# Kernel optimization log

Measured on AMD Instinct MI355X. Metric: run time of the kernel, lower is better.

## Reference

```python
import jax, jax.numpy as jnp
import numpy as np
import math

B, T, C, H = 8, 1024, 1024, 16
HS = C // H  # head size 64
FF = 4 * C
EPS = 1e-5


def quant_weight(W, e, b):
    """Fake-quant with straight-through rounding, per QLinear.forward.
    W:[...,out,in], e:[...,out,1], b:[...,out,1] -> effective weight 2**e * round_ste(clip(2**-e * W))."""
    b_rel = jax.nn.relu(b)
    mn = jnp.where(b_rel > 0, -(2.0 ** (b_rel - 1)), 0.0)
    mx = jnp.where(b_rel > 0, 2.0 ** (b_rel - 1) - 1.0, 0.0)
    qw = jnp.clip((2.0 ** (-e)) * W, mn, mx)
    w = qw + jax.lax.stop_gradient(jnp.round(qw) - qw)  # STE round
    return (2.0 ** e) * w


def layer_norm(x, g, beta):
    mu = jnp.mean(x, axis=-1, keepdims=True)
    var = jnp.mean((x - mu) ** 2, axis=-1, keepdims=True)
    return (x - mu) * jax.lax.rsqrt(var + EPS) * g + beta


def _uniform(key, shape, fan_in):
    s = 1.0 / math.sqrt(fan_in)
    return jax.random.uniform(key, shape, jnp.float32, -s, s)


def setup_inputs() -> dict:
    key = jax.random.key(0)
    ks = jax.random.split(key, 8)
    d = {"x": jax.random.normal(ks[0], (B, T, C), jnp.float32)}
    # stacked per-head QKV QLinear params (bias=False)
    d["Wq"] = _uniform(ks[1], (H, HS, C), C)
    d["Wk"] = _uniform(ks[2], (H, HS, C), C)
    d["Wv"] = _uniform(ks[3], (H, HS, C), C)
    for n in ("q", "k", "v"):
        d["e" + n] = jnp.full((H, HS, 1), -8.0, jnp.float32)
        d["b" + n] = jnp.full((H, HS, 1), 32.0, jnp.float32)
    # output projection QLinear (bias=True)
    d["Wp"] = _uniform(ks[4], (C, C), C)
    d["ep"] = jnp.full((C, 1), -8.0, jnp.float32)
    d["bp"] = jnp.full((C, 1), 32.0, jnp.float32)
    d["biasp"] = jnp.zeros((C,), jnp.float32)
    # FFN QLinears
    d["W1"] = _uniform(ks[5], (FF, C), C)
    d["e1"] = jnp.full((FF, 1), -8.0, jnp.float32)
    d["b1"] = jnp.full((FF, 1), 32.0, jnp.float32)
    d["bias1"] = jnp.zeros((FF,), jnp.float32)
    d["W2"] = _uniform(ks[6], (C, FF), FF)
    d["e2"] = jnp.full((C, 1), -8.0, jnp.float32)
    d["b2"] = jnp.full((C, 1), 32.0, jnp.float32)
    d["bias2"] = jnp.zeros((C,), jnp.float32)
    # LayerNorms
    d["g1"] = jnp.ones((C,), jnp.float32)
    d["be1"] = jnp.zeros((C,), jnp.float32)
    d["g2"] = jnp.ones((C,), jnp.float32)
    d["be2"] = jnp.zeros((C,), jnp.float32)
    return d


def block_forward(x, Wq, eq, bq, Wk, ek, bk, Wv, ev, bv,
                  Wp, ep, bp, biasp, W1, e1, b1, bias1, W2, e2, b2, bias2,
                  g1, be1, g2, be2):
    h = layer_norm(x, g1, be1)
    q = jnp.einsum('btc,hdc->bhtd', h, quant_weight(Wq, eq, bq))
    k = jnp.einsum('btc,hdc->bhtd', h, quant_weight(Wk, ek, bk))
    v = jnp.einsum('btc,hdc->bhtd', h, quant_weight(Wv, ev, bv))
    # NOTE: source scales by C**-0.5 where C = n_embd (not head_size)
    wei = jnp.einsum('bhtd,bhsd->bhts', q, k) * (C ** -0.5)
    causal = jnp.tril(jnp.ones((T, T), bool))
    wei = jnp.where(causal, wei, -jnp.inf)
    wei = jax.nn.softmax(wei, axis=-1)
    att = jnp.einsum('bhts,bhsd->bhtd', wei, v)  # [B,H,T,HS]
    att = att.transpose(0, 2, 1, 3).reshape(B, T, C)  # concat heads
    x = x + att @ quant_weight(Wp, ep, bp).T + biasp
    h2 = layer_norm(x, g2, be2)
    f = jax.nn.relu(h2 @ quant_weight(W1, e1, b1).T + bias1)
    f = f @ quant_weight(W2, e2, b2).T + bias2
    return x + f


def reference(x, Wq, eq, bq, Wk, ek, bk, Wv, ev, bv,
              Wp, ep, bp, biasp, W1, e1, b1, bias1, W2, e2, b2, bias2,
              g1, be1, g2, be2):
    return block_forward(x, Wq, eq, bq, Wk, ek, bk, Wv, ev, bv,
                         Wp, ep, bp, biasp, W1, e1, b1, bias1, W2, e2, b2, bias2,
                         g1, be1, g2, be2)
```

## Files before the change

### kernel.cpp

```cpp
#include <hip/hip_runtime.h>
#include <hip/hip_bf16.h>
#include <math.h>

#define DEVI __device__ __forceinline__

typedef __attribute__((ext_vector_type(8))) short bf16x8;
typedef __attribute__((ext_vector_type(4))) float f32x4;

DEVI unsigned short f2bf(float f) {
    union { float f; unsigned u; } v; v.f = f;
    unsigned r = v.u + 0x7FFFu + ((v.u >> 16) & 1u);
    return (unsigned short)(r >> 16);
}

DEVI unsigned cvtpk(float lo, float hi) {
    unsigned d;
    asm volatile("v_cvt_pk_bf16_f32 %0, %1, %2" : "=v"(d) : "v"(lo), "v"(hi));
    return d;
}

DEVI void gload16(const void* g, void* l) {
    __builtin_amdgcn_global_load_lds((const __attribute__((address_space(1))) void*)g,
                                     (__attribute__((address_space(3))) void*)l, 16, 0, 0);
}

#define WAITVM8() asm volatile("s_waitcnt vmcnt(8)" ::: "memory")
#define WAITVM4() asm volatile("s_waitcnt vmcnt(4)" ::: "memory")
#define WAITVM0() asm volatile("s_waitcnt vmcnt(0)" ::: "memory")
#define WAITLG0() asm volatile("s_waitcnt lgkmcnt(0)" ::: "memory")
#define WAITLG8() asm volatile("s_waitcnt lgkmcnt(8)" ::: "memory")
#define BAR()     __builtin_amdgcn_s_barrier()
#define SB()      __builtin_amdgcn_sched_barrier(0)

__global__ __launch_bounds__(256) void quant6_kernel(
    const float* __restrict__ Wq, const float* __restrict__ Wk, const float* __restrict__ Wv,
    const float* __restrict__ Wp, const float* __restrict__ W1, const float* __restrict__ W2,
    const float* __restrict__ eq, const float* __restrict__ ek, const float* __restrict__ ev,
    const float* __restrict__ ep, const float* __restrict__ e1, const float* __restrict__ e2,
    const float* __restrict__ bq, const float* __restrict__ bk, const float* __restrict__ bv,
    const float* __restrict__ bp, const float* __restrict__ b1, const float* __restrict__ b2,
    unsigned short* __restrict__ Wqkvq, unsigned short* __restrict__ Wpq,
    unsigned short* __restrict__ W1q, unsigned short* __restrict__ W2q)
{
    const int M1 = 1 << 20;
    const int NCH = 3 * M1;
    for (int c = blockIdx.x * blockDim.x + threadIdx.x; c < NCH; c += gridDim.x * blockDim.x) {
        int elem = c * 4;
        const float *W, *e, *b; unsigned short* o; int lgK, local;
        if (elem < M1)            { W = Wq; e = eq; b = bq; o = Wqkvq;          lgK = 10; local = elem; }
        else if (elem < 2 * M1)   { W = Wk; e = ek; b = bk; o = Wqkvq + M1;     lgK = 10; local = elem - M1; }
        else if (elem < 3 * M1)   { W = Wv; e = ev; b = bv; o = Wqkvq + 2 * M1; lgK = 10; local = elem - 2 * M1; }
        else if (elem < 4 * M1)   { W = Wp; e = ep; b = bp; o = Wpq;            lgK = 10; local = elem - 3 * M1; }
        else if (elem < 8 * M1)   { W = W1; e = e1; b = b1; o = W1q;            lgK = 10; local = elem - 4 * M1; }
        else                      { W = W2; e = e2; b = b2; o = W2q;            lgK = 12; local = elem - 8 * M1; }
        int row = local >> lgK;
        float evv = e[row], bvv = b[row];
        float br = fmaxf(bvv, 0.f);
        float mn, mx;
        if (br > 0.f) { float p = exp2f(br - 1.f); mn = -p; mx = p - 1.f; }
        else          { mn = 0.f; mx = 0.f; }
        float si = exp2f(-evv), so = exp2f(evv);
        union { float4 v4; float a[4]; } v;
        v.v4 = *(const float4*)(W + local);
        union { unsigned short u[4]; unsigned long long ll; } ot;
        #pragma unroll
        for (int j = 0; j < 4; j++) {
            float qw = fminf(fmaxf(si * v.a[j], mn), mx);
            ot.u[j] = f2bf(so * rintf(qw));
        }
        *(unsigned long long*)(o + local) = ot.ll;
    }
}

__global__ __launch_bounds__(256) void ln_kernel(
    const float* __restrict__ x, const float* __restrict__ g, const float* __restrict__ be,
    unsigned short* __restrict__ out)
{
    int row = blockIdx.x;
    union { float4 v4; float a[4]; } v;
    v.v4 = ((const float4*)(x + (size_t)row * 1024))[threadIdx.x];
    float s = v.a[0] + v.a[1] + v.a[2] + v.a[3];
    float s2 = v.a[0]*v.a[0] + v.a[1]*v.a[1] + v.a[2]*v.a[2] + v.a[3]*v.a[3];
    #pragma unroll
    for (int off = 32; off > 0; off >>= 1) { s += __shfl_down(s, off); s2 += __shfl_down(s2, off); }
    __shared__ float ps[4], ps2[4];
    int wave = threadIdx.x >> 6, lane = threadIdx.x & 63;
    if (lane == 0) { ps[wave] = s; ps2[wave] = s2; }
    __syncthreads();
    float mu = (ps[0] + ps[1] + ps[2] + ps[3]) * (1.0f / 1024.0f);
    float var = (ps2[0] + ps2[1] + ps2[2] + ps2[3]) * (1.0f / 1024.0f) - mu * mu;
    float rs = rsqrtf(var + 1e-5f);
    int c = threadIdx.x * 4;
    union { unsigned short u[4]; unsigned long long ll; } o;
    #pragma unroll
    for (int j = 0; j < 4; j++) o.u[j] = f2bf((v.a[j] - mu) * rs * g[c + j] + be[c + j]);
    *(unsigned long long*)(out + (size_t)row * 1024 + c) = o.ll;
}

#define GSTAGE(buf, kt) do { \
    _Pragma("unroll") for (int q_ = 0; q_ < 4; q_++) { \
        int idx_ = q_ * 256 + tid; int row_ = idx_ >> 3; int gs_ = (idx_ & 7) ^ (row_ & 7); \
        gload16(A  + (size_t)(brow + row_) * K + (kt) * 64 + gs_ * 8, &As[buf][idx_ * 8]); \
        gload16(Bw + (size_t)(bcol + row_) * K + (kt) * 64 + gs_ * 8, &Bs[buf][idx_ * 8]); \
    } } while (0)

template<int EP>
__global__ __launch_bounds__(256) void gemm_bt(
    const unsigned short* __restrict__ A, const unsigned short* __restrict__ Bw,
    int N, int K,
    const float* __restrict__ bias, const float* __restrict__ res,
    float* __restrict__ outf, unsigned short* __restrict__ outb)
{
    __shared__ __align__(16) unsigned short As[2][128 * 64];
    __shared__ __align__(16) unsigned short Bs[2][128 * 64];
    int tid = threadIdx.x, lane = tid & 63, wave = tid >> 6;
    int gx = gridDim.x;
    int nwg = gx * gridDim.y;
    int id = blockIdx.y * gx + blockIdx.x;
    int swz = (id & 7) * (nwg >> 3) + (id >> 3);
    int brow = (swz / gx) * 128, bcol = (swz % gx) * 128;
    int wr = wave >> 1, wc = wave & 1;
    int r = lane & 15, g4 = lane >> 4;
    f32x4 acc[4][4];
    #pragma unroll
    for (int i = 0; i < 4; i++)
        #pragma unroll
        for (int j = 0; j < 4; j++) acc[i][j] = (f32x4){0.f, 0.f, 0.f, 0.f};

    int nt = K >> 6;
    GSTAGE(0, 0);
    __syncthreads();
    int cur = 0;
    for (int t = 0; t < nt; ++t) {
        if (t + 1 < nt) { GSTAGE(cur ^ 1, t + 1); WAITVM8(); }
        else            { WAITVM0(); }
        __builtin_amdgcn_s_barrier();
        #pragma unroll
        for (int kk = 0; kk < 2; kk++) {
            bf16x8 af[4], bfr[4];
            #pragma unroll
            for (int mi = 0; mi < 4; mi++) {
                int rh = wr * 64 + mi * 16 + r;
                af[mi] = *(const bf16x8*)&As[cur][rh * 64 + (((kk * 4 + g4) ^ (rh & 7)) << 3)];
            }
            #pragma unroll
            for (int ni = 0; ni < 4; ni++) {
                int rh = wc * 64 + ni * 16 + r;
                bfr[ni] = *(const bf16x8*)&Bs[cur][rh * 64 + (((kk * 4 + g4) ^ (rh & 7)) << 3)];
            }
            #pragma unroll
            for (int mi = 0; mi < 4; mi++)
                #pragma unroll
                for (int ni = 0; ni < 4; ni++)
                    acc[mi][ni] = __builtin_amdgcn_mfma_f32_16x16x32_bf16(af[mi], bfr[ni], acc[mi][ni], 0, 0, 0);
        }
        __builtin_amdgcn_s_barrier();
        cur ^= 1;
    }

    #pragma unroll
    for (int mi = 0; mi < 4; mi++)
        #pragma unroll
        for (int ni = 0; ni < 4; ni++)
            #pragma unroll
            for (int i = 0; i < 4; i++) {
                int row = brow + wr * 64 + mi * 16 + g4 * 4 + i;
                int col = bcol + wc * 64 + ni * 16 + r;
                float v = acc[mi][ni][i];
                if (EP == 0) {
                    outb[(size_t)row * N + col] = f2bf(v);
                } else if (EP == 1) {
                    outf[(size_t)row * N + col] = v + bias[col] + res[(size_t)row * N + col];
                } else {
                    outb[(size_t)row * N + col] = f2bf(fmaxf(v + bias[col], 0.f));
                }
            }
}

#define STAGE_A(b, h, kt) do { \
    _Pragma("unroll") \
    for (int ld = 0; ld < 2; ld++) { \
        int idx = ld * 512 + tid; int rw = idx >> 3; int gs = (idx & 7) ^ (rw & 7); \
        gload16(Aa + (size_t)(brow + (h) * 128 + rw) * K + (kt) * 64 + gs * 8, &As[b][h][idx * 8]); \
    } } while (0)

#define STAGE_B(b, h, kt) do { \
    _Pragma("unroll") \
    for (int ld = 0; ld < 2; ld++) { \
        int idx = ld * 512 + tid; int rw = idx >> 3; int gs = (idx & 7) ^ (rw & 7); \
        gload16(Bw + (size_t)(bcol + (h) * 128 + rw) * K + (kt) * 64 + gs * 8, &Bs[b][h][idx * 8]); \
    } } while (0)

#define RD_A(b, mh) do { \
    _Pragma("unroll") for (int mi = 0; mi < 4; mi++) \
    _Pragma("unroll") for (int kk = 0; kk < 2; kk++) { \
        int rh = (mh) * 64 + mi * 16 + r; \
        af[mi][kk] = *(const bf16x8*)&As[b][wr][rh * 64 + (((kk * 4 + g4) ^ (rh & 7)) << 3)]; \
    } } while (0)

#define RD_B2(b, nh) do { \
    _Pragma("unroll") for (int nj = 0; nj < 2; nj++) \
    _Pragma("unroll") for (int kk = 0; kk < 2; kk++) { \
        int rh = (wc & 1) * 64 + ((nh) * 2 + nj) * 16 + r; \
        bfr[(nh) * 2 + nj][kk] = *(const bf16x8*)&Bs[b][wc >> 1][rh * 64 + (((kk * 4 + g4) ^ (rh & 7)) << 3)]; \
    } } while (0)

#define QUAD(mh, nh) do { \
    __builtin_amdgcn_s_setprio(1); \
    _Pragma("unroll") for (int mi = 0; mi < 4; mi++) \
    _Pragma("unroll") for (int nj = 0; nj < 2; nj++) \
    _Pragma("unroll") for (int kk = 0; kk < 2; kk++) \
        acc[(mh) * 4 + mi][(nh) * 2 + nj] = __builtin_amdgcn_mfma_f32_16x16x32_bf16( \
            af[mi][kk], bfr[(nh) * 2 + nj][kk], acc[(mh) * 4 + mi][(nh) * 2 + nj], 0, 0, 0); \
    __builtin_amdgcn_s_setprio(0); \
    } while (0)

template<int EP>
__global__ __launch_bounds__(512, 2) void gemm256(
    const unsigned short* __restrict__ Aa, const unsigned short* __restrict__ Bw,
    int N, int K,
    const float* __restrict__ bias, const float* __restrict__ res,
    float* __restrict__ outf, unsigned short* __restrict__ outb)
{
    __shared__ __align__(16) unsigned short As[2][2][128 * 64];
    __shared__ __align__(16) unsigned short Bs[2][2][128 * 64];
    int tid = threadIdx.x, lane = tid & 63, wave = tid >> 6;
    int gx = gridDim.x;
    int nwg = gx * gridDim.y;
    int id = blockIdx.y * gx + blockIdx.x;
    int swz = (id & 7) * (nwg >> 3) + (id >> 3);
    int brow = (swz / gx) * 256, bcol = (swz % gx) * 256;
    int wr = wave >> 2, wc = wave & 3;
    int r = lane & 15, g4 = lane >> 4;
    int KT = K >> 6;

    f32x4 acc[8][4];
    #pragma unroll
    for (int i = 0; i < 8; i++)
        #pragma unroll
        for (int j = 0; j < 4; j++) acc[i][j] = (f32x4){0.f, 0.f, 0.f, 0.f};
    bf16x8 af[4][2], bfr[4][2];

    STAGE_A(0, 0, 0); STAGE_A(0, 1, 0); STAGE_B(0, 0, 0); STAGE_B(0, 1, 0);
    STAGE_B(1, 0, 1); STAGE_B(1, 1, 1);
    WAITVM4();
    BAR();

    for (int t = 0; t < KT; t += 2) {
        RD_A(0, 0); RD_B2(0, 0);
        STAGE_A(1, 0, t + 1);
        WAITLG8();
        BAR(); WAITLG0(); SB();
        QUAD(0, 0);
        BAR();
        RD_B2(0, 1);
        STAGE_A(1, 1, t + 1);
        BAR(); WAITLG0(); SB();
        QUAD(0, 1);
        BAR();
        RD_A(0, 1);
        if (t + 2 < KT) STAGE_B(0, 0, t + 2);
        BAR(); WAITLG0(); SB();
        QUAD(1, 1);
        BAR();
        if (t + 2 < KT) { STAGE_B(0, 1, t + 2); WAITVM4(); } else { WAITVM0(); }
        BAR(); WAITLG0(); SB();
        QUAD(1, 0);
        BAR();
        RD_A(1, 0); RD_B2(1, 0);
        if (t + 2 < KT) STAGE_A(0, 0, t + 2);
        WAITLG8();
        BAR(); WAITLG0(); SB();
        QUAD(0, 0);
        BAR();
        RD_B2(1, 1);
        if (t + 2 < KT) STAGE_A(0, 1, t + 2);
        BAR(); WAITLG0(); SB();
        QUAD(0, 1);
        BAR();
        RD_A(1, 1);
        if (t + 3 < KT) STAGE_B(1, 0, t + 3);
        BAR(); WAITLG0(); SB();
        QUAD(1, 1);
        BAR();
        if (t + 3 < KT) { STAGE_B(1, 1, t + 3); WAITVM4(); } else { WAITVM0(); }
        BAR(); WAITLG0(); SB();
        QUAD(1, 0);
        BAR();
    }

    #pragma unroll
    for (int m = 0; m < 8; m++)
        #pragma unroll
        for (int n = 0; n < 4; n++)
            #pragma unroll
            for (int j = 0; j < 4; j++) {
                int row = brow + wr * 128 + m * 16 + g4 * 4 + j;
                int col = bcol + wc * 64 + n * 16 + r;
                float v = acc[m][n][j];
                if (EP == 0) {
                    outb[(size_t)row * N + col] = f2bf(v);
                } else if (EP == 1) {
                    outf[(size_t)row * N + col] = v + bias[col] + res[(size_t)row * N + col];
                } else {
                    outb[(size_t)row * N + col] = f2bf(fmaxf(v + bias[col], 0.f));
                }
            }
}

__global__ __launch_bounds__(512, 4) void attn_kernel(
    const unsigned short* __restrict__ qkv, unsigned short* __restrict__ att)
{
    __shared__ __align__(16) unsigned short Ks[2][64 * 64];
    __shared__ __align__(16) unsigned short Vt[2][64 * 66];
    __shared__ __align__(16) unsigned short Ps[2][64 * 64];
    int tid = threadIdx.x, lane = tid & 63, w = tid >> 6;
    int half = w >> 2;
    int pi = blockIdx.x;
    int bh = blockIdx.y, bb = bh >> 4, hh = bh & 15;
    int r = lane & 15, g4 = lane >> 4;
    const unsigned short* base = qkv + (size_t)bb * 1024 * 3072;
    const float SCL = 0.03125f * 1.4426950408889634f;
    int vd = tid & 63, vsb = tid >> 6;
    int prow = (w & 3) * 16 + r;
    int pswz = (r & 7) << 3;

    for (int sidx = 0; sidx < 2; sidx++) {
        int s = sidx ? (7 - pi) : pi;
        int qt = 2 * s + half;
        int qtmax = 2 * s + 1;
        int qrow = qt * 64 + prow;

        bf16x8 qf[2];
        #pragma unroll
        for (int kk = 0; kk < 2; kk++)
            qf[kk] = *(const bf16x8*)&base[(size_t)qrow * 3072 + hh * 64 + kk * 32 + g4 * 8];

        f32x4 oacc[4];
        #pragma unroll
        for (int i = 0; i < 4; i++) oacc[i] = (f32x4){0.f, 0.f, 0.f, 0.f};
        float m_i = -INFINITY, l_i = 0.f;

        unsigned short vtmp[8];
        {
            int row = tid >> 3, slot = tid & 7;
            int gs = slot ^ (row & 7);
            gload16(base + (size_t)row * 3072 + 1024 + hh * 64 + gs * 8, &Ks[0][tid * 8]);
            #pragma unroll
            for (int i2 = 0; i2 < 8; i2++)
                vtmp[i2] = base[(size_t)(vsb * 8 + i2) * 3072 + 2048 + hh * 64 + vd];
            union { unsigned short u[8]; bf16x8 v; } w0;
            #pragma unroll
            for (int i2 = 0; i2 < 8; i2++) w0.u[i2] = vtmp[i2];
            *(bf16x8*)&Vt[0][vd * 66 + (vsb ^ (vd & 7)) * 8] = w0.v;
        }
        __syncthreads();

        for (int ki = 0; ki <= qtmax; ki++) {
            int cur = ki & 1;
            bool pre = (ki < qtmax);
            bool act = (ki <= qt);
            if (pre) {
                int k1 = (ki + 1) * 64;
                int row = tid >> 3, slot = tid & 7;
                int gs = slot ^ (row & 7);
                gload16(base + (size_t)(k1 + row) * 3072 + 1024 + hh * 64 + gs * 8, &Ks[cur ^ 1][tid * 8]);
                #pragma unroll
                for (int i2 = 0; i2 < 8; i2++)
                    vtmp[i2] = base[(size_t)(k1 + vsb * 8 + i2) * 3072 + 2048 + hh * 64 + vd];
            }

            if (act) {
                int k0 = ki * 64;
                f32x4 sacc[4];
                #pragma unroll
                for (int c4 = 0; c4 < 4; c4++) sacc[c4] = (f32x4){0.f, 0.f, 0.f, 0.f};
                #pragma unroll
                for (int c4 = 0; c4 < 4; c4++) {
                    int krow = c4 * 16 + r;
                    #pragma unroll
                    for (int kk = 0; kk < 2; kk++) {
                        int slot = (g4 + kk * 4) ^ (krow & 7);
                        bf16x8 kf = *(const bf16x8*)&Ks[cur][krow * 64 + slot * 8];
                        sacc[c4] = __builtin_amdgcn_mfma_f32_16x16x32_bf16(kf, qf[kk], sacc[c4], 0, 0, 0);
                    }
                }
                bool diag = (ki == qt);
                float sv[4][4];
                float smax = -INFINITY;
                #pragma unroll
                for (int c4 = 0; c4 < 4; c4++)
                    #pragma unroll
                    for (int i = 0; i < 4; i++) {
                        float sa = sacc[c4][i];
                        if (diag && (k0 + c4 * 16 + g4 * 4 + i) > qrow) sa = -INFINITY;
                        sv[c4][i] = sa;
                        smax = fmaxf(smax, sa);
                    }
                smax = fmaxf(smax, __shfl_xor(smax, 16));
                smax = fmaxf(smax, __shfl_xor(smax, 32));
                if (!__all((smax - m_i) * SCL <= 8.f)) {
                    float mn = fmaxf(m_i, smax);
                    float fs = exp2f((m_i - mn) * SCL);
                    m_i = mn;
                    l_i *= fs;
                    #pragma unroll
                    for (int n4 = 0; n4 < 4; n4++)
                        #pragma unroll
                        for (int i = 0; i < 4; i++) oacc[n4][i] *= fs;
                }
                float nb = -m_i * SCL;
                float rsum = 0.f;
                float pv[4][4];
                #pragma unroll
                for (int c4 = 0; c4 < 4; c4++)
                    #pragma unroll
                    for (int i = 0; i < 4; i++) {
                        float p = exp2f(fmaf(sv[c4][i], SCL, nb));
                        pv[c4][i] = p;
                        rsum += p;
                    }
                rsum += __shfl_xor(rsum, 16);
                rsum += __shfl_xor(rsum, 32);
                l_i += rsum;
                #pragma unroll
                for (int c4 = 0; c4 < 4; c4++) {
                    unsigned long long ll = (unsigned long long)cvtpk(pv[c4][0], pv[c4][1])
                                          | ((unsigned long long)cvtpk(pv[c4][2], pv[c4][3]) << 32);
                    *(unsigned long long*)&Ps[half][(prow * 64 + c4 * 16 + g4 * 4) ^ pswz] = ll;
                }
                WAITLG0();
            }
            if (pre) {
                union { unsigned short u[8]; bf16x8 v; } w0;
                #pragma unroll
                for (int i2 = 0; i2 < 8; i2++) w0.u[i2] = vtmp[i2];
                *(bf16x8*)&Vt[cur ^ 1][vd * 66 + (vsb ^ (vd & 7)) * 8] = w0.v;
            }
            if (act) {
                bf16x8 pa[2];
                #pragma unroll
                for (int kk = 0; kk < 2; kk++)
                    pa[kk] = *(const bf16x8*)&Ps[half][(prow * 64 + kk * 32 + g4 * 8) ^ pswz];
                #pragma unroll
                for (int n4 = 0; n4 < 4; n4++) {
                    int d = n4 * 16 + r;
                    #pragma unroll
                    for (int kk = 0; kk < 2; kk++) {
                        bf16x8 vf = *(const bf16x8*)&Vt[cur][d * 66 + (((kk * 4 + g4) ^ (d & 7)) << 3)];
                        oacc[n4] = __builtin_amdgcn_mfma_f32_16x16x32_bf16(vf, pa[kk], oacc[n4], 0, 0, 0);
                    }
                }
            }
            __syncthreads();
        }

        float inv = 1.f / l_i;
        #pragma unroll
        for (int n4 = 0; n4 < 4; n4++) {
            unsigned long long ll = (unsigned long long)cvtpk(oacc[n4][0] * inv, oacc[n4][1] * inv)
                                  | ((unsigned long long)cvtpk(oacc[n4][2] * inv, oacc[n4][3] * inv) << 32);
            size_t oidx = ((size_t)(bb * 1024 + qrow)) * 1024 + hh * 64 + n4 * 16 + g4 * 4;
            *(unsigned long long*)&att[oidx] = ll;
        }
    }
}

extern "C" void kernel_launch(void* const* d_in, const int* in_sizes, int n_in,
                              void* d_out, int out_size, void* d_ws, size_t ws_size,
                              hipStream_t stream)
{
    const float* x     = (const float*)d_in[0];
    const float* Wq    = (const float*)d_in[1];
    const float* Wk    = (const float*)d_in[2];
    const float* Wv    = (const float*)d_in[3];
    const float* eq    = (const float*)d_in[4];
    const float* bq    = (const float*)d_in[5];
    const float* ek    = (const float*)d_in[6];
    const float* bk    = (const float*)d_in[7];
    const float* ev    = (const float*)d_in[8];
    const float* bv    = (const float*)d_in[9];
    const float* Wp    = (const float*)d_in[10];
    const float* ep    = (const float*)d_in[11];
    const float* bp    = (const float*)d_in[12];
    const float* biasp = (const float*)d_in[13];
    const float* W1    = (const float*)d_in[14];
    const float* e1    = (const float*)d_in[15];
    const float* b1    = (const float*)d_in[16];
    const float* bias1 = (const float*)d_in[17];
    const float* W2    = (const float*)d_in[18];
    const float* e2    = (const float*)d_in[19];
    const float* b2    = (const float*)d_in[20];
    const float* bias2 = (const float*)d_in[21];
    const float* g1    = (const float*)d_in[22];
    const float* be1   = (const float*)d_in[23];
    const float* g2    = (const float*)d_in[24];
    const float* be2   = (const float*)d_in[25];

    const size_t MB = 1ull << 20;
    char* ws = (char*)d_ws;
    unsigned short* Wqkvq = (unsigned short*)(ws);
    unsigned short* Wpq   = (unsigned short*)(ws + 6 * MB);
    unsigned short* W1q   = (unsigned short*)(ws + 8 * MB);
    unsigned short* W2q   = (unsigned short*)(ws + 16 * MB);
    unsigned short* hbuf  = (unsigned short*)(ws + 24 * MB);
    unsigned short* qkvb  = (unsigned short*)(ws + 40 * MB);
    unsigned short* fbuf  = qkvb;
    unsigned short* attb  = (unsigned short*)(ws + 88 * MB);
    float*          x2    = (float*)(ws + 104 * MB);

    quant6_kernel<<<2048, 256, 0, stream>>>(Wq, Wk, Wv, Wp, W1, W2,
                                            eq, ek, ev, ep, e1, e2,
                                            bq, bk, bv, bp, b1, b2,
                                            Wqkvq, Wpq, W1q, W2q);

    ln_kernel<<<8192, 256, 0, stream>>>(x, g1, be1, hbuf);
    gemm256<0><<<dim3(12, 32), 512, 0, stream>>>(hbuf, Wqkvq, 3072, 1024, nullptr, nullptr, nullptr, qkvb);
    attn_kernel<<<dim3(4, 128), 512, 0, stream>>>(qkvb, attb);
    gemm_bt<1><<<dim3(8, 64), 256, 0, stream>>>(attb, Wpq, 1024, 1024, biasp, x, x2, nullptr);
    ln_kernel<<<8192, 256, 0, stream>>>(x2, g2, be2, hbuf);
    gemm256<2><<<dim3(16, 32), 512, 0, stream>>>(hbuf, W1q, 4096, 1024, bias1, nullptr, nullptr, fbuf);
    gemm_bt<1><<<dim3(8, 64), 256, 0, stream>>>(fbuf, W2q, 1024, 4096, bias2, x2, (float*)d_out, nullptr);
}
```

Baseline: 329.1 us.

## Fuse weight quant with first LayerNorm, store residual x2 in bf16

```diff
diff --git a/kernel.cpp b/kernel.cpp
--- a/kernel.cpp
+++ b/kernel.cpp
@@ -11,6 +11,10 @@
     union { float f; unsigned u; } v; v.f = f;
     unsigned r = v.u + 0x7FFFu + ((v.u >> 16) & 1u);
     return (unsigned short)(r >> 16);
+}
+
+DEVI float bf2f(unsigned short u) {
+    union { unsigned u; float f; } v; v.u = (unsigned)u << 16; return v.f;
 }
 
 DEVI unsigned cvtpk(float lo, float hi) {
@@ -32,7 +36,7 @@
 #define BAR()     __builtin_amdgcn_s_barrier()
 #define SB()      __builtin_amdgcn_sched_barrier(0)
 
-__global__ __launch_bounds__(256) void quant6_kernel(
+__global__ __launch_bounds__(256) void fused_pre_kernel(
     const float* __restrict__ Wq, const float* __restrict__ Wk, const float* __restrict__ Wv,
     const float* __restrict__ Wp, const float* __restrict__ W1, const float* __restrict__ W2,
     const float* __restrict__ eq, const float* __restrict__ ek, const float* __restrict__ ev,
@@ -40,61 +44,103 @@
     const float* __restrict__ bq, const float* __restrict__ bk, const float* __restrict__ bv,
     const float* __restrict__ bp, const float* __restrict__ b1, const float* __restrict__ b2,
     unsigned short* __restrict__ Wqkvq, unsigned short* __restrict__ Wpq,
-    unsigned short* __restrict__ W1q, unsigned short* __restrict__ W2q)
+    unsigned short* __restrict__ W1q, unsigned short* __restrict__ W2q,
+    const float* __restrict__ x, const float* __restrict__ g1, const float* __restrict__ be1,
+    unsigned short* __restrict__ hbuf)
 {
     const int M1 = 1 << 20;
-    const int NCH = 3 * M1;
-    for (int c = blockIdx.x * blockDim.x + threadIdx.x; c < NCH; c += gridDim.x * blockDim.x) {
-        int elem = c * 4;
-        const float *W, *e, *b; unsigned short* o; int lgK, local;
-        if (elem < M1)            { W = Wq; e = eq; b = bq; o = Wqkvq;          lgK = 10; local = elem; }
-        else if (elem < 2 * M1)   { W = Wk; e = ek; b = bk; o = Wqkvq + M1;     lgK = 10; local = elem - M1; }
-        else if (elem < 3 * M1)   { W = Wv; e = ev; b = bv; o = Wqkvq + 2 * M1; lgK = 10; local = elem - 2 * M1; }
-        else if (elem < 4 * M1)   { W = Wp; e = ep; b = bp; o = Wpq;            lgK = 10; local = elem - 3 * M1; }
-        else if (elem < 8 * M1)   { W = W1; e = e1; b = b1; o = W1q;            lgK = 10; local = elem - 4 * M1; }
-        else                      { W = W2; e = e2; b = b2; o = W2q;            lgK = 12; local = elem - 8 * M1; }
-        int row = local >> lgK;
-        float evv = e[row], bvv = b[row];
-        float br = fmaxf(bvv, 0.f);
-        float mn, mx;
-        if (br > 0.f) { float p = exp2f(br - 1.f); mn = -p; mx = p - 1.f; }
-        else          { mn = 0.f; mx = 0.f; }
-        float si = exp2f(-evv), so = exp2f(evv);
-        union { float4 v4; float a[4]; } v;
-        v.v4 = *(const float4*)(W + local);
-        union { unsigned short u[4]; unsigned long long ll; } ot;
+    if (blockIdx.x < 2048) {
+        const int NCH = 3 * M1;
+        const int STRIDE = 2048 * 256;
+        for (int c = blockIdx.x * blockDim.x + threadIdx.x; c < NCH; c += STRIDE) {
+            int elem = c * 4;
+            const float *W, *e, *b; unsigned short* o; int lgK, local;
+            if (elem < M1)            { W = Wq; e = eq; b = bq; o = Wqkvq;          lgK = 10; local = elem; }
+            else if (elem < 2 * M1)   { W = Wk; e = ek; b = bk; o = Wqkvq + M1;     lgK = 10; local = elem - M1; }
+            else if (elem < 3 * M1)   { W = Wv; e = ev; b = bv; o = Wqkvq + 2 * M1; lgK = 10; local = elem - 2 * M1; }
+            else if (elem < 4 * M1)   { W = Wp; e = ep; b = bp; o = Wpq;            lgK = 10; local = elem - 3 * M1; }
+            else if (elem < 8 * M1)   { W = W1; e = e1; b = b1; o = W1q;            lgK = 10; local = elem - 4 * M1; }
+            else                      { W = W2; e = e2; b = b2; o = W2q;            lgK = 12; local = elem - 8 * M1; }
+            int row = local >> lgK;
+            float evv = e[row], bvv = b[row];
+            float br = fmaxf(bvv, 0.f);
+            float mn, mx;
+            if (br > 0.f) { float p = exp2f(br - 1.f); mn = -p; mx = p - 1.f; }
+            else          { mn = 0.f; mx = 0.f; }
+            float si = exp2f(-evv), so = exp2f(evv);
+            union { float4 v4; float a[4]; } v;
+            v.v4 = *(const float4*)(W + local);
+            union { unsigned short u[4]; unsigned long long ll; } ot;
+            #pragma unroll
+            for (int j = 0; j < 4; j++) {
+                float qw = fminf(fmaxf(si * v.a[j], mn), mx);
+                ot.u[j] = f2bf(so * rintf(qw));
+            }
+            *(unsigned long long*)(o + local) = ot.ll;
+        }
+    } else {
+        int row = (blockIdx.x - 2048) * 4 + (threadIdx.x >> 6);
+        int lane = threadIdx.x & 63;
+        const float* xp = x + (size_t)row * 1024 + lane * 16;
+        float a[16];
         #pragma unroll
         for (int j = 0; j < 4; j++) {
-            float qw = fminf(fmaxf(si * v.a[j], mn), mx);
-            ot.u[j] = f2bf(so * rintf(qw));
+            float4 v = *(const float4*)(xp + j * 4);
+            a[j * 4] = v.x; a[j * 4 + 1] = v.y; a[j * 4 + 2] = v.z; a[j * 4 + 3] = v.w;
         }
-        *(unsigned long long*)(o + local) = ot.ll;
+        float s = 0.f, s2 = 0.f;
+        #pragma unroll
+        for (int i = 0; i < 16; i++) { s += a[i]; s2 += a[i] * a[i]; }
+        #pragma unroll
+        for (int off = 1; off < 64; off <<= 1) { s += __shfl_xor(s, off); s2 += __shfl_xor(s2, off); }
+        float mu = s * (1.0f / 1024.0f);
+        float var = s2 * (1.0f / 1024.0f) - mu * mu;
+        float rs = rsqrtf(var + 1e-5f);
+        int c0 = lane * 16;
+        float r[16];
+        #pragma unroll
+        for (int i = 0; i < 16; i++) r[i] = (a[i] - mu) * rs * g1[c0 + i] + be1[c0 + i];
+        unsigned w[8];
+        #pragma unroll
+        for (int j = 0; j < 8; j++) w[j] = cvtpk(r[2 * j], r[2 * j + 1]);
+        unsigned short* op = hbuf + (size_t)row * 1024 + c0;
+        *(uint4*)(op)     = *(uint4*)&w[0];
+        *(uint4*)(op + 8) = *(uint4*)&w[4];
     }
 }
 
-__global__ __launch_bounds__(256) void ln_kernel(
-    const float* __restrict__ x, const float* __restrict__ g, const float* __restrict__ be,
+__global__ __launch_bounds__(256) void ln_bf_kernel(
+    const unsigned short* __restrict__ xb, const float* __restrict__ g, const float* __restrict__ be,
     unsigned short* __restrict__ out)
 {
-    int row = blockIdx.x;
-    union { float4 v4; float a[4]; } v;
-    v.v4 = ((const float4*)(x + (size_t)row * 1024))[threadIdx.x];
-    float s = v.a[0] + v.a[1] + v.a[2] + v.a[3];
-    float s2 = v.a[0]*v.a[0] + v.a[1]*v.a[1] + v.a[2]*v.a[2] + v.a[3]*v.a[3];
-    #pragma unroll
-    for (int off = 32; off > 0; off >>= 1) { s += __shfl_down(s, off); s2 += __shfl_down(s2, off); }
-    __shared__ float ps[4], ps2[4];
-    int wave = threadIdx.x >> 6, lane = threadIdx.x & 63;
-    if (lane == 0) { ps[wave] = s; ps2[wave] = s2; }
-    __syncthreads();
-    float mu = (ps[0] + ps[1] + ps[2] + ps[3]) * (1.0f / 1024.0f);
-    float var = (ps2[0] + ps2[1] + ps2[2] + ps2[3]) * (1.0f / 1024.0f) - mu * mu;
+    int row = blockIdx.x * 4 + (threadIdx.x >> 6);
+    int lane = threadIdx.x & 63;
+    const unsigned short* xp = xb + (size_t)row * 1024 + lane * 16;
+    float a[16];
+    #pragma unroll
+    for (int j = 0; j < 2; j++) {
+        bf16x8 v = *(const bf16x8*)(xp + j * 8);
+        #pragma unroll
+        for (int i = 0; i < 8; i++) a[j * 8 + i] = bf2f(((unsigned short*)&v)[i]);
+    }
+    float s = 0.f, s2 = 0.f;
+    #pragma unroll
+    for (int i = 0; i < 16; i++) { s += a[i]; s2 += a[i] * a[i]; }
+    #pragma unroll
+    for (int off = 1; off < 64; off <<= 1) { s += __shfl_xor(s, off); s2 += __shfl_xor(s2, off); }
+    float mu = s * (1.0f / 1024.0f);
+    float var = s2 * (1.0f / 1024.0f) - mu * mu;
     float rs = rsqrtf(var + 1e-5f);
-    int c = threadIdx.x * 4;
-    union { unsigned short u[4]; unsigned long long ll; } o;
-    #pragma unroll
-    for (int j = 0; j < 4; j++) o.u[j] = f2bf((v.a[j] - mu) * rs * g[c + j] + be[c + j]);
-    *(unsigned long long*)(out + (size_t)row * 1024 + c) = o.ll;
+    int c0 = lane * 16;
+    float r[16];
+    #pragma unroll
+    for (int i = 0; i < 16; i++) r[i] = (a[i] - mu) * rs * g[c0 + i] + be[c0 + i];
+    unsigned w[8];
+    #pragma unroll
+    for (int j = 0; j < 8; j++) w[j] = cvtpk(r[2 * j], r[2 * j + 1]);
+    unsigned short* op = out + (size_t)row * 1024 + c0;
+    *(uint4*)(op)     = *(uint4*)&w[0];
+    *(uint4*)(op + 8) = *(uint4*)&w[4];
 }
 
 #define GSTAGE(buf, kt) do { \
@@ -109,6 +155,7 @@
     const unsigned short* __restrict__ A, const unsigned short* __restrict__ Bw,
     int N, int K,
     const float* __restrict__ bias, const float* __restrict__ res,
+    const unsigned short* __restrict__ resb,
     float* __restrict__ outf, unsigned short* __restrict__ outb)
 {
     __shared__ __align__(16) unsigned short As[2][128 * 64];
@@ -171,8 +218,12 @@
                     outb[(size_t)row * N + col] = f2bf(v);
                 } else if (EP == 1) {
                     outf[(size_t)row * N + col] = v + bias[col] + res[(size_t)row * N + col];
+                } else if (EP == 2) {
+                    outb[(size_t)row * N + col] = f2bf(fmaxf(v + bias[col], 0.f));
+                } else if (EP == 3) {
+                    outb[(size_t)row * N + col] = f2bf(v + bias[col] + res[(size_t)row * N + col]);
                 } else {
-                    outb[(size_t)row * N + col] = f2bf(fmaxf(v + bias[col], 0.f));
+                    outf[(size_t)row * N + col] = v + bias[col] + bf2f(resb[(size_t)row * N + col]);
                 }
             }
 }
@@ -507,18 +558,18 @@
     unsigned short* qkvb  = (unsigned short*)(ws + 40 * MB);
     unsigned short* fbuf  = qkvb;
     unsigned short* attb  = (unsigned short*)(ws + 88 * MB);
-    float*          x2    = (float*)(ws + 104 * MB);
-
-    quant6_kernel<<<2048, 256, 0, stream>>>(Wq, Wk, Wv, Wp, W1, W2,
-                                            eq, ek, ev, ep, e1, e2,
-                                            bq, bk, bv, bp, b1, b2,
-                                            Wqkvq, Wpq, W1q, W2q);
-
-    ln_kernel<<<8192, 256, 0, stream>>>(x, g1, be1, hbuf);
+    unsigned short* x2b   = (unsigned short*)(ws + 104 * MB);
+
+    fused_pre_kernel<<<4096, 256, 0, stream>>>(Wq, Wk, Wv, Wp, W1, W2,
+                                               eq, ek, ev, ep, e1, e2,
+                                               bq, bk, bv, bp, b1, b2,
+                                               Wqkvq, Wpq, W1q, W2q,
+                                               x, g1, be1, hbuf);
+
     gemm256<0><<<dim3(12, 32), 512, 0, stream>>>(hbuf, Wqkvq, 3072, 1024, nullptr, nullptr, nullptr, qkvb);
     attn_kernel<<<dim3(4, 128), 512, 0, stream>>>(qkvb, attb);
-    gemm_bt<1><<<dim3(8, 64), 256, 0, stream>>>(attb, Wpq, 1024, 1024, biasp, x, x2, nullptr);
-    ln_kernel<<<8192, 256, 0, stream>>>(x2, g2, be2, hbuf);
+    gemm_bt<3><<<dim3(8, 64), 256, 0, stream>>>(attb, Wpq, 1024, 1024, biasp, x, nullptr, nullptr, x2b);
+    ln_bf_kernel<<<2048, 256, 0, stream>>>(x2b, g2, be2, hbuf);
     gemm256<2><<<dim3(16, 32), 512, 0, stream>>>(hbuf, W1q, 4096, 1024, bias1, nullptr, nullptr, fbuf);
-    gemm_bt<1><<<dim3(8, 64), 256, 0, stream>>>(fbuf, W2q, 1024, 4096, bias2, x2, (float*)d_out, nullptr);
-}
+    gemm_bt<4><<<dim3(8, 64), 256, 0, stream>>>(fbuf, W2q, 1024, 4096, bias2, nullptr, x2b, (float*)d_out, nullptr);
+}
```

New measurement: 322.3 us. 1.02x faster.
